# Kernel tuning notes

Hardware: AMD Instinct MI355X
Metric: run time of the kernel (lower is better)

The kernel has to match this reference:

```python
import jax, jax.numpy as jnp
import numpy as np

B, S, E = 4, 2048, 1024

def setup_inputs() -> dict:
    key = jax.random.key(0)
    ks = jax.random.split(key, 9)
    lim = 1.0 / np.sqrt(E)
    inp = {
        "query": jax.random.normal(ks[0], (B, S, E), dtype=jnp.float32),
        "key": jax.random.normal(ks[1], (B, S, E), dtype=jnp.float32),
        "value": jax.random.normal(ks[2], (B, S, E), dtype=jnp.float32),
        "Wq": jax.random.uniform(ks[3], (E, E), jnp.float32, -lim, lim),
        "bq": jax.random.uniform(ks[4], (E,), jnp.float32, -lim, lim),
        "Wk": jax.random.uniform(ks[5], (E, E), jnp.float32, -lim, lim),
        "bk": jax.random.uniform(ks[6], (E,), jnp.float32, -lim, lim),
        "Wv": jax.random.uniform(ks[7], (E, E), jnp.float32, -lim, lim),
        "bv": jax.random.uniform(ks[8], (E,), jnp.float32, -lim, lim),
    }
    return inp

def reference(query, key, value, Wq, bq, Wk, bk, Wv, bv):
    # Linear layers (torch stores weight as [out,in]; here W is [in,out] used as x @ W)
    q = query @ Wq + bq            # [B,S,E]
    k = key @ Wk + bk              # [B,S,E]
    v = value @ Wv + bv            # [B,S,E]
    inv_scale = jnp.asarray(E, q.dtype) ** 0.5
    scores = jnp.einsum("bse,bte->bst", q, k) / inv_scale  # [B,S,S]
    attn = jax.nn.softmax(scores, axis=-1)
    # dropout_p = 0.0 -> identity
    out = jnp.einsum("bst,bte->bse", attn, v)  # [B,S,E]
    return out
```

## Files before the change

kernel.cpp:

```cpp
#include <hip/hip_runtime.h>
#include <hip/hip_bf16.h>


typedef __bf16 bf16_t;
typedef bf16_t bf16x8 __attribute__((ext_vector_type(8)));
typedef bf16_t bf16x4 __attribute__((ext_vector_type(4)));
typedef float  f32x4  __attribute__((ext_vector_type(4)));

typedef const __attribute__((address_space(1))) unsigned gl_uint;
typedef __attribute__((address_space(3))) unsigned lds_uint;

#define BM 128
#define BN 128
#define BK 64

__device__ __forceinline__ void gload_lds16(const void* g, void* l) {
  __builtin_amdgcn_global_load_lds((gl_uint*)g, (lds_uint*)l, 16, 0, 0);
}

template <bool LSUM>
__device__ __forceinline__ void mfma_tile(const bf16_t* As, const bf16_t* Bs,
                                          f32x4 acc[4][4], f32x4 acc_l[4]) {
  const int lane = threadIdx.x & 63;
  const int quad = lane >> 4;
  const int l15  = lane & 15;
  const int wid  = threadIdx.x >> 6;
  const int wm   = (wid >> 1) * 64;
  const int wn   = (wid & 1) * 64;
  const int csw  = l15 & 7;
  bf16x8 ones;
  if (LSUM) {
#pragma unroll
    for (int t = 0; t < 8; ++t) ones[t] = (bf16_t)1.0f;
  }
#pragma unroll
  for (int ks = 0; ks < 2; ++ks) {
    const int sg = ks * 4 + quad;
    const int c  = (sg ^ csw) * 8;
    bf16x8 fa[4], fb[4];
#pragma unroll
    for (int i = 0; i < 4; ++i)
      fa[i] = *(const bf16x8*)&As[(wm + i * 16 + l15) * BK + c];
#pragma unroll
    for (int i = 0; i < 4; ++i)
      fb[i] = *(const bf16x8*)&Bs[(wn + i * 16 + l15) * BK + c];
#pragma unroll
    for (int mi = 0; mi < 4; ++mi)
#pragma unroll
      for (int ni = 0; ni < 4; ++ni)
        acc[mi][ni] = __builtin_amdgcn_mfma_f32_16x16x32_bf16(
            fa[mi], fb[ni], acc[mi][ni], 0, 0, 0);
    if (LSUM) {
#pragma unroll
      for (int mi = 0; mi < 4; ++mi)
        acc_l[mi] = __builtin_amdgcn_mfma_f32_16x16x32_bf16(
            fa[mi], ones, acc_l[mi], 0, 0, 0);
    }
  }
}

template <bool LSUM>
__device__ __forceinline__ void gemm_core_bf16(
    const bf16_t* __restrict__ Ab, const bf16_t* __restrict__ Bb,
    const int K, bf16_t* As, bf16_t* Bs, f32x4 acc[4][4], f32x4 acc_l[4])
{
  const int tid = threadIdx.x;
  for (int kt = 0; kt < K; kt += BK) {
#pragma unroll
    for (int j = 0; j < 4; ++j) {
      const int lin = j * 256 + tid;
      const int row = lin >> 3;
      const int seg = (lin & 7) ^ (row & 7);
      gload_lds16(Ab + (size_t)row * K + kt + seg * 8, &As[lin * 8]);
    }
#pragma unroll
    for (int j = 0; j < 4; ++j) {
      const int lin = j * 256 + tid;
      const int row = lin >> 3;
      const int seg = (lin & 7) ^ (row & 7);
      gload_lds16(Bb + (size_t)row * K + kt + seg * 8, &Bs[lin * 8]);
    }
    __syncthreads();
    mfma_tile<LSUM>(As, Bs, acc, acc_l);
    __syncthreads();
  }
}

__global__ __launch_bounds__(256, 2)
void qkv_proj(const bf16_t* __restrict__ qb, const bf16_t* __restrict__ kb,
              const bf16_t* __restrict__ vb, const bf16_t* __restrict__ Wqt,
              const bf16_t* __restrict__ Wkt, const bf16_t* __restrict__ Wvt,
              const float* __restrict__ bq, const float* __restrict__ bk,
              const float* __restrict__ bv, bf16_t* __restrict__ qp,
              bf16_t* __restrict__ kp, bf16_t* __restrict__ vT)
{
  __shared__ __align__(16) bf16_t As[BM * BK];
  __shared__ __align__(16) bf16_t Bs[BN * BK];

  const int L = blockIdx.x;
  const int g = L >> 3;
  const int gst = (L & 7) * 3 + (g >> 6);
  const int z  = gst >> 3;
  const int sy = gst & 7;
  const int w  = g & 63;
  const int bx = w & 7;
  const int by = sy * 8 + (w >> 3);

  const bf16_t* A    = (z == 0) ? qb : (z == 1) ? kb : vb;
  const bf16_t* W    = (z == 0) ? Wqt : (z == 1) ? Wkt : Wvt;
  const float*  bias = (z == 0) ? bq : (z == 1) ? bk : bv;
  const int K = 1024, N = 1024;
  const bf16_t* Ab = A + (size_t)by * BM * K;
  const bf16_t* Bb = W + (size_t)bx * BN * K;

  f32x4 acc[4][4];
  const f32x4 z4 = {0.f, 0.f, 0.f, 0.f};
#pragma unroll
  for (int i = 0; i < 4; ++i)
#pragma unroll
    for (int j = 0; j < 4; ++j) acc[i][j] = z4;

  gemm_core_bf16<false>(Ab, Bb, K, As, Bs, acc, nullptr);

  const int lane = threadIdx.x & 63;
  const int quad = lane >> 4;
  const int l15  = lane & 15;
  const int wid  = threadIdx.x >> 6;
  const int wm = (wid >> 1) * 64, wn = (wid & 1) * 64;
  const int m0 = by * BM, n0 = bx * BN;
#pragma unroll
  for (int mi = 0; mi < 4; ++mi) {
#pragma unroll
    for (int ni = 0; ni < 4; ++ni) {
      const int gn = n0 + wn + ni * 16 + l15;
      const int gm = m0 + wm + mi * 16 + quad * 4;
      const float bv_ = bias[gn];
      f32x4 a = acc[mi][ni];
      if (z < 2) {
        bf16_t* C = (z == 0) ? qp : kp;
#pragma unroll
        for (int r = 0; r < 4; ++r)
          C[(size_t)(gm + r) * N + gn] = (bf16_t)(a[r] + bv_);
      } else {
        const int b = gm >> 11;
        const int s = gm & 2047;
        bf16x4 o;
#pragma unroll
        for (int r = 0; r < 4; ++r) o[r] = (bf16_t)(a[r] + bv_);
        *(bf16x4*)&vT[((size_t)b * N + gn) * 2048 + s] = o;
      }
    }
  }
}

template <int MODE>
__global__ __launch_bounds__(256, 2)
void gemm_att(const bf16_t* __restrict__ A, const bf16_t* __restrict__ Bt,
              void* __restrict__ Cv,
              const int M, const int N, const int K,
              const long long sA, const long long sB, const long long sC)
{
  __shared__ __align__(16) bf16_t As[BM * BK];
  __shared__ __align__(16) bf16_t Bs[BN * BK];

  const int L = blockIdx.x;
  int bx, by, bz;
  if (MODE == 0) {
    const int g = L >> 3;
    const int gst = (L & 7) * 2 + (g >> 6);
    bz = gst >> 2;
    const int s2 = gst & 3;
    const int w = g & 63;
    bx = (s2 & 1) * 8 + (w & 7);
    by = (s2 >> 1) * 8 + (w >> 3);
  } else {
    const int xcd = L & 7;
    const int w = (L >> 3) & 63;
    bz = xcd >> 1;
    bx = w & 7;
    by = (xcd & 1) * 8 + (w >> 3);
  }

  const bf16_t* Ab = A + (size_t)bz * sA + (size_t)by * BM * K;
  const bf16_t* Bb = Bt + (size_t)bz * sB + (size_t)bx * BN * K;

  f32x4 acc[4][4];
  f32x4 acc_l[4];
  const f32x4 z4 = {0.f, 0.f, 0.f, 0.f};
#pragma unroll
  for (int i = 0; i < 4; ++i) {
    acc_l[i] = z4;
#pragma unroll
    for (int j = 0; j < 4; ++j) acc[i][j] = z4;
  }

  gemm_core_bf16<MODE == 1>(Ab, Bb, K, As, Bs, acc, acc_l);

  const int lane = threadIdx.x & 63;
  const int quad = lane >> 4;
  const int l15  = lane & 15;
  const int wid  = threadIdx.x >> 6;
  const int wm = (wid >> 1) * 64, wn = (wid & 1) * 64;
  const int m0 = by * BM, n0 = bx * BN;

  if (MODE == 0) {
    const float cexp = 0.03125f * 1.4426950408889634f;
    bf16_t* C = (bf16_t*)Cv + (size_t)bz * sC;
#pragma unroll
    for (int mi = 0; mi < 4; ++mi) {
      const int gm = m0 + wm + mi * 16 + quad * 4;
#pragma unroll
      for (int ni = 0; ni < 4; ++ni) {
        const int gn = n0 + wn + ni * 16 + l15;
        f32x4 a = acc[mi][ni];
#pragma unroll
        for (int r = 0; r < 4; ++r)
          C[(size_t)(gm + r) * N + gn] = (bf16_t)exp2f(a[r] * cexp);
      }
    }
  } else {
    float* C = (float*)Cv + (size_t)bz * sC;
#pragma unroll
    for (int mi = 0; mi < 4; ++mi) {
      const int gm = m0 + wm + mi * 16 + quad * 4;
      float il[4];
#pragma unroll
      for (int r = 0; r < 4; ++r) il[r] = 1.0f / acc_l[mi][r];
#pragma unroll
      for (int ni = 0; ni < 4; ++ni) {
        const int gn = n0 + wn + ni * 16 + l15;
        f32x4 a = acc[mi][ni];
#pragma unroll
        for (int r = 0; r < 4; ++r)
          C[(size_t)(gm + r) * N + gn] = a[r] * il[r];
      }
    }
  }
}

__global__ __launch_bounds__(256)
void prep(const float* __restrict__ q, const float* __restrict__ k,
          const float* __restrict__ v, const float* __restrict__ Wq,
          const float* __restrict__ Wk, const float* __restrict__ Wv,
          bf16_t* __restrict__ qo, bf16_t* __restrict__ ko,
          bf16_t* __restrict__ vo, bf16_t* __restrict__ Wqt,
          bf16_t* __restrict__ Wkt, bf16_t* __restrict__ Wvt) {
  const int L = blockIdx.x;
  const int tid = threadIdx.x;
  if (L < 24576) {
    const int z = L >> 13;
    const int blk = L & 8191;
    const float* in = (z == 0) ? q : (z == 1) ? k : v;
    bf16_t* out = (z == 0) ? qo : (z == 1) ? ko : vo;
    const size_t i = ((size_t)blk * 256 + tid) * 4;
    const float4 w = *(const float4*)(in + i);
    bf16x4 o;
    o[0] = (bf16_t)w.x; o[1] = (bf16_t)w.y; o[2] = (bf16_t)w.z; o[3] = (bf16_t)w.w;
    *(bf16x4*)(out + i) = o;
  } else {
    const int t = L - 24576;
    const int z = t >> 8;
    const int wi = t & 255;
    const float* W = (z == 0) ? Wq : (z == 1) ? Wk : Wv;
    bf16_t* Wt = (z == 0) ? Wqt : (z == 1) ? Wkt : Wvt;
    __shared__ float tile[64][65];
    const int n0 = (wi & 15) * 64;
    const int k0 = (wi >> 4) * 64;
#pragma unroll
    for (int it = 0; it < 16; ++it) {
      const int idx = it * 256 + tid;
      const int r = idx >> 6, c = idx & 63;
      tile[r][c] = W[(size_t)(k0 + r) * 1024 + n0 + c];
    }
    __syncthreads();
#pragma unroll
    for (int it = 0; it < 16; ++it) {
      const int idx = it * 256 + tid;
      const int r = idx >> 6, c = idx & 63;
      Wt[(size_t)(n0 + r) * 1024 + k0 + c] = (bf16_t)tile[c][r];
    }
  }
}

extern "C" void kernel_launch(void* const* d_in, const int* in_sizes, int n_in,
                              void* d_out, int out_size, void* d_ws, size_t ws_size,
                              hipStream_t stream) {
  const int B = 4, S = 2048, E = 1024;
  const size_t BSE = (size_t)B * S * E;
  const size_t EE  = (size_t)E * E;

  const float* q_in = (const float*)d_in[0];
  const float* k_in = (const float*)d_in[1];
  const float* v_in = (const float*)d_in[2];
  const float* Wq = (const float*)d_in[3];
  const float* bq = (const float*)d_in[4];
  const float* Wk = (const float*)d_in[5];
  const float* bk = (const float*)d_in[6];
  const float* Wv = (const float*)d_in[7];
  const float* bv = (const float*)d_in[8];
  float* out = (float*)d_out;

  char* ws = (char*)d_ws;
  bf16_t* Wqt = (bf16_t*)ws;
  bf16_t* Wkt = Wqt + EE;
  bf16_t* Wvt = Wkt + EE;
  bf16_t* qb  = Wvt + EE;
  bf16_t* kb  = qb + BSE;
  bf16_t* vb  = kb + BSE;
  bf16_t* qp  = vb + BSE;
  bf16_t* kp  = qp + BSE;
  bf16_t* vT  = kp + BSE;
  bf16_t* P   = vT + BSE;

  prep<<<25344, 256, 0, stream>>>(q_in, k_in, v_in, Wq, Wk, Wv,
                                  qb, kb, vb, Wqt, Wkt, Wvt);

  qkv_proj<<<1536, 256, 0, stream>>>(qb, kb, vb, Wqt, Wkt, Wvt,
                                     bq, bk, bv, qp, kp, vT);

  gemm_att<0><<<1024, 256, 0, stream>>>(
      qp, kp, P, S, S, E,
      (long long)S * E, (long long)S * E, (long long)S * S);

  gemm_att<1><<<512, 256, 0, stream>>>(
      P, vT, out, S, E, S,
      (long long)S * S, (long long)E * S, (long long)S * E);

  (void)in_sizes; (void)n_in; (void)out_size; (void)ws_size;
}
```

Before: 285.1 us.

## Use 256x256 eight-wave pipelined GEMM for QKV projection and scores

Adds a 256x256-tile GEMM core for 8 waves. It double-buffers LDS with direct global-to-LDS loads, uses explicit vmcnt waits, barriers and setprio so loads overlap the MFMA phases. The QKV projection and score kernels switch to this core with fewer, larger blocks, and the scores epilogue writes exp2 of the scaled scores directly to P. Larger tiles raise data reuse and cut global traffic, but they use more registers and 128KB of LDS, and a smaller grid risks poorer load balance across CUs. The scores epilogue has no max subtraction, so it relies on the score range staying small enough for exp without overflow.

```diff
diff --git a/kernel.cpp b/kernel.cpp
--- a/kernel.cpp
+++ b/kernel.cpp
@@ -16,6 +16,231 @@
 
 __device__ __forceinline__ void gload_lds16(const void* g, void* l) {
   __builtin_amdgcn_global_load_lds((gl_uint*)g, (lds_uint*)l, 16, 0, 0);
+}
+
+#define VMCNT(N) asm volatile("s_waitcnt vmcnt(" #N ")" ::: "memory")
+#define LGKM0()  asm volatile("s_waitcnt lgkmcnt(0)" ::: "memory")
+
+__device__ __forceinline__ void gemm256_8p(
+    const bf16_t* __restrict__ Ab, const bf16_t* __restrict__ Bb,
+    const int K, bf16_t* Lb, f32x4 acc[8][4])
+{
+  const int tid  = threadIdx.x;
+  const int lane = tid & 63;
+  const int l15  = lane & 15;
+  const int quad = lane >> 4;
+  const int wid  = tid >> 6;
+  const int wr   = wid >> 2;
+  const int wc   = wid & 3;
+  const int swz0 = (quad ^ (l15 & 7)) * 8;
+  const int swz1 = ((quad + 4) ^ (l15 & 7)) * 8;
+
+  const int r0  = tid >> 3, r1 = r0 + 64;
+  const int so0 = r0 * K + (((tid & 7) ^ (r0 & 7)) * 8);
+  const int so1 = r1 * K + (((tid & 7) ^ (r1 & 7)) * 8);
+  const int sd0 = tid * 8, sd1 = 4096 + tid * 8;
+
+#define HALF(buf, h) (Lb + ((buf) * 4 + (h)) * 8192)
+#define STAGE(gsrc, buf, h) { const bf16_t* _g = (gsrc); bf16_t* _l = HALF(buf, h); \
+    gload_lds16(_g + so0, _l + sd0); gload_lds16(_g + so1, _l + sd1); }
+
+  const int aoff = l15 * 64;
+  const int boff = ((wc & 1) * 64 + l15) * 64;
+  bf16x8 fa[4][2], fb[4][2];
+
+#define RD_FB(buf) { const bf16_t* _B = HALF(buf, 2 + (wc >> 1)) + boff; \
+  _Pragma("unroll") for (int ni = 0; ni < 4; ++ni) { \
+    fb[ni][0] = *(const bf16x8*)(_B + ni * 1024 + swz0); \
+    fb[ni][1] = *(const bf16x8*)(_B + ni * 1024 + swz1); } }
+#define RD_FA(buf, MO) { const bf16_t* _A = HALF(buf, wr) + aoff + (MO) * 1024; \
+  _Pragma("unroll") for (int mi = 0; mi < 4; ++mi) { \
+    fa[mi][0] = *(const bf16x8*)(_A + mi * 1024 + swz0); \
+    fa[mi][1] = *(const bf16x8*)(_A + mi * 1024 + swz1); } }
+
+#define MFQ(MH, NL) \
+  _Pragma("unroll") for (int kk = 0; kk < 2; ++kk) \
+  _Pragma("unroll") for (int mi = 0; mi < 4; ++mi) \
+  _Pragma("unroll") for (int ni = 0; ni < 2; ++ni) \
+    acc[(MH) * 4 + mi][(NL) + ni] = __builtin_amdgcn_mfma_f32_16x16x32_bf16( \
+        fa[mi][kk], fb[(NL) + ni][kk], acc[(MH) * 4 + mi][(NL) + ni], 0, 0, 0);
+
+#define PH_PRE() __builtin_amdgcn_s_barrier(); LGKM0(); \
+                 __builtin_amdgcn_sched_barrier(0); __builtin_amdgcn_s_setprio(1)
+#define PH_POST() __builtin_amdgcn_s_setprio(0); __builtin_amdgcn_sched_barrier(0)
+
+  const int NJ = K >> 7;
+  const size_t hk = (size_t)128 * K;
+
+  STAGE(Bb,           0, 2);  STAGE(Bb + hk,      0, 3);
+  STAGE(Ab,           0, 0);  STAGE(Ab + hk,      0, 1);
+  STAGE(Bb + 64,      1, 2);  STAGE(Bb + hk + 64, 1, 3);
+  STAGE(Ab + 64,      1, 0);
+  VMCNT(6);
+  __builtin_amdgcn_s_barrier();
+
+  for (int j = 0; j < NJ - 1; ++j) {
+    const int c1 = 2 * j * 64 + 64;
+    const int c2 = c1 + 64, c3 = c2 + 64;
+    RD_FB(0); RD_FA(0, 0);
+    STAGE(Ab + hk + c1, 1, 1);
+    PH_PRE(); MFQ(0, 0); PH_POST(); __builtin_amdgcn_s_barrier();
+    STAGE(Bb + c2, 0, 2);
+    PH_PRE(); MFQ(0, 2); PH_POST(); __builtin_amdgcn_s_barrier();
+    RD_FA(0, 4);
+    STAGE(Bb + hk + c2, 0, 3);
+    PH_PRE(); MFQ(1, 0); PH_POST(); __builtin_amdgcn_s_barrier();
+    STAGE(Ab + c2, 0, 0);
+    PH_PRE(); MFQ(1, 2); PH_POST(); VMCNT(6); __builtin_amdgcn_s_barrier();
+    RD_FB(1); RD_FA(1, 0);
+    STAGE(Ab + hk + c2, 0, 1);
+    PH_PRE(); MFQ(0, 0); PH_POST(); __builtin_amdgcn_s_barrier();
+    STAGE(Bb + c3, 1, 2);
+    PH_PRE(); MFQ(0, 2); PH_POST(); __builtin_amdgcn_s_barrier();
+    RD_FA(1, 4);
+    STAGE(Bb + hk + c3, 1, 3);
+    PH_PRE(); MFQ(1, 0); PH_POST(); __builtin_amdgcn_s_barrier();
+    STAGE(Ab + c3, 1, 0);
+    PH_PRE(); MFQ(1, 2); PH_POST(); VMCNT(6); __builtin_amdgcn_s_barrier();
+  }
+  {
+    const int c1 = K - 64;
+    RD_FB(0); RD_FA(0, 0);
+    STAGE(Ab + hk + c1, 1, 1);
+    PH_PRE(); MFQ(0, 0); PH_POST(); __builtin_amdgcn_s_barrier();
+    PH_PRE(); MFQ(0, 2); PH_POST(); __builtin_amdgcn_s_barrier();
+    RD_FA(0, 4);
+    PH_PRE(); MFQ(1, 0); PH_POST(); __builtin_amdgcn_s_barrier();
+    PH_PRE(); MFQ(1, 2); PH_POST(); VMCNT(0); __builtin_amdgcn_s_barrier();
+    RD_FB(1); RD_FA(1, 0);
+    PH_PRE(); MFQ(0, 0); PH_POST(); __builtin_amdgcn_s_barrier();
+    PH_PRE(); MFQ(0, 2); PH_POST(); __builtin_amdgcn_s_barrier();
+    RD_FA(1, 4);
+    PH_PRE(); MFQ(1, 0); PH_POST(); __builtin_amdgcn_s_barrier();
+    PH_PRE(); MFQ(1, 2); PH_POST();
+  }
+#undef HALF
+#undef STAGE
+#undef RD_FB
+#undef RD_FA
+#undef MFQ
+#undef PH_PRE
+#undef PH_POST
+}
+
+__global__ __launch_bounds__(512, 2)
+void qkv_proj8(const bf16_t* __restrict__ qb, const bf16_t* __restrict__ kb,
+               const bf16_t* __restrict__ vb, const bf16_t* __restrict__ Wqt,
+               const bf16_t* __restrict__ Wkt, const bf16_t* __restrict__ Wvt,
+               const float* __restrict__ bq, const float* __restrict__ bk,
+               const float* __restrict__ bv, bf16_t* __restrict__ qp,
+               bf16_t* __restrict__ kp, bf16_t* __restrict__ vT)
+{
+  __shared__ __align__(16) bf16_t lds[2 * 4 * 8192];
+  const int L   = blockIdx.x;
+  const int lin = (L & 7) * 48 + (L >> 3);
+  const int z   = lin >> 7;
+  const int r   = lin & 127;
+  const int by  = r >> 2, bx = r & 3;
+  const int K = 1024, N = 1024;
+
+  const bf16_t* A    = (z == 0) ? qb : (z == 1) ? kb : vb;
+  const bf16_t* W    = (z == 0) ? Wqt : (z == 1) ? Wkt : Wvt;
+  const float*  bias = (z == 0) ? bq : (z == 1) ? bk : bv;
+
+  f32x4 acc[8][4];
+  const f32x4 z4 = {0.f, 0.f, 0.f, 0.f};
+#pragma unroll
+  for (int i = 0; i < 8; ++i)
+#pragma unroll
+    for (int jj = 0; jj < 4; ++jj) acc[i][jj] = z4;
+
+  gemm256_8p(A + (size_t)by * 256 * K, W + (size_t)bx * 256 * K, K, lds, acc);
+
+  const int tid = threadIdx.x;
+  const int lane = tid & 63, l15 = lane & 15, quad = lane >> 4;
+  const int wid = tid >> 6, wr = wid >> 2, wc = wid & 3;
+  const int m0 = by * 256 + wr * 128;
+  const int n0 = bx * 256 + wc * 64;
+  float bv_[4];
+#pragma unroll
+  for (int ni = 0; ni < 4; ++ni) bv_[ni] = bias[n0 + ni * 16 + l15];
+
+  if (z < 2) {
+    bf16_t* C = (z == 0) ? qp : kp;
+#pragma unroll
+    for (int mi = 0; mi < 8; ++mi) {
+      const int gm = m0 + mi * 16 + quad * 4;
+#pragma unroll
+      for (int ni = 0; ni < 4; ++ni) {
+        const int gn = n0 + ni * 16 + l15;
+        f32x4 a = acc[mi][ni];
+#pragma unroll
+        for (int rr = 0; rr < 4; ++rr)
+          C[(size_t)(gm + rr) * N + gn] = (bf16_t)(a[rr] + bv_[ni]);
+      }
+    }
+  } else {
+#pragma unroll
+    for (int mi = 0; mi < 8; ++mi) {
+      const int gm = m0 + mi * 16 + quad * 4;
+      const int b = gm >> 11;
+      const int s = gm & 2047;
+#pragma unroll
+      for (int ni = 0; ni < 4; ++ni) {
+        const int gn = n0 + ni * 16 + l15;
+        f32x4 a = acc[mi][ni];
+        bf16x4 o;
+#pragma unroll
+        for (int rr = 0; rr < 4; ++rr) o[rr] = (bf16_t)(a[rr] + bv_[ni]);
+        *(bf16x4*)&vT[((size_t)b * N + gn) * 2048 + s] = o;
+      }
+    }
+  }
+}
+
+__global__ __launch_bounds__(512, 2)
+void scores8(const bf16_t* __restrict__ qp, const bf16_t* __restrict__ kp,
+             bf16_t* __restrict__ P)
+{
+  __shared__ __align__(16) bf16_t lds[2 * 4 * 8192];
+  const int L   = blockIdx.x;
+  const int lin = (L & 7) * 32 + (L >> 3);
+  const int bz  = lin >> 6;
+  const int r   = lin & 63;
+  const int by  = r >> 3, bx = r & 7;
+  const int K = 1024;
+
+  const bf16_t* Ab = qp + (size_t)bz * 2048 * 1024 + (size_t)by * 256 * K;
+  const bf16_t* Bb = kp + (size_t)bz * 2048 * 1024 + (size_t)bx * 256 * K;
+
+  f32x4 acc[8][4];
+  const f32x4 z4 = {0.f, 0.f, 0.f, 0.f};
+#pragma unroll
+  for (int i = 0; i < 8; ++i)
+#pragma unroll
+    for (int jj = 0; jj < 4; ++jj) acc[i][jj] = z4;
+
+  gemm256_8p(Ab, Bb, K, lds, acc);
+
+  const int tid = threadIdx.x;
+  const int lane = tid & 63, l15 = lane & 15, quad = lane >> 4;
+  const int wid = tid >> 6, wr = wid >> 2, wc = wid & 3;
+  const int m0 = by * 256 + wr * 128;
+  const int n0 = bx * 256 + wc * 64;
+  bf16_t* C = P + (size_t)bz * 2048 * 2048;
+  const float cexp = 0.03125f * 1.4426950408889634f;
+#pragma unroll
+  for (int mi = 0; mi < 8; ++mi) {
+    const int gm = m0 + mi * 16 + quad * 4;
+#pragma unroll
+    for (int ni = 0; ni < 4; ++ni) {
+      const int gn = n0 + ni * 16 + l15;
+      f32x4 a = acc[mi][ni];
+#pragma unroll
+      for (int rr = 0; rr < 4; ++rr)
+        C[(size_t)(gm + rr) * 2048 + gn] = (bf16_t)exp2f(a[rr] * cexp);
+    }
+  }
 }
 
 template <bool LSUM>
@@ -83,73 +308,6 @@
     __syncthreads();
     mfma_tile<LSUM>(As, Bs, acc, acc_l);
     __syncthreads();
-  }
-}
-
-__global__ __launch_bounds__(256, 2)
-void qkv_proj(const bf16_t* __restrict__ qb, const bf16_t* __restrict__ kb,
-              const bf16_t* __restrict__ vb, const bf16_t* __restrict__ Wqt,
-              const bf16_t* __restrict__ Wkt, const bf16_t* __restrict__ Wvt,
-              const float* __restrict__ bq, const float* __restrict__ bk,
-              const float* __restrict__ bv, bf16_t* __restrict__ qp,
-              bf16_t* __restrict__ kp, bf16_t* __restrict__ vT)
-{
-  __shared__ __align__(16) bf16_t As[BM * BK];
-  __shared__ __align__(16) bf16_t Bs[BN * BK];
-
-  const int L = blockIdx.x;
-  const int g = L >> 3;
-  const int gst = (L & 7) * 3 + (g >> 6);
-  const int z  = gst >> 3;
-  const int sy = gst & 7;
-  const int w  = g & 63;
-  const int bx = w & 7;
-  const int by = sy * 8 + (w >> 3);
-
-  const bf16_t* A    = (z == 0) ? qb : (z == 1) ? kb : vb;
-  const bf16_t* W    = (z == 0) ? Wqt : (z == 1) ? Wkt : Wvt;
-  const float*  bias = (z == 0) ? bq : (z == 1) ? bk : bv;
-  const int K = 1024, N = 1024;
-  const bf16_t* Ab = A + (size_t)by * BM * K;
-  const bf16_t* Bb = W + (size_t)bx * BN * K;
-
-  f32x4 acc[4][4];
-  const f32x4 z4 = {0.f, 0.f, 0.f, 0.f};
-#pragma unroll
-  for (int i = 0; i < 4; ++i)
-#pragma unroll
-    for (int j = 0; j < 4; ++j) acc[i][j] = z4;
-
-  gemm_core_bf16<false>(Ab, Bb, K, As, Bs, acc, nullptr);
-
-  const int lane = threadIdx.x & 63;
-  const int quad = lane >> 4;
-  const int l15  = lane & 15;
-  const int wid  = threadIdx.x >> 6;
-  const int wm = (wid >> 1) * 64, wn = (wid & 1) * 64;
-  const int m0 = by * BM, n0 = bx * BN;
-#pragma unroll
-  for (int mi = 0; mi < 4; ++mi) {
-#pragma unroll
-    for (int ni = 0; ni < 4; ++ni) {
-      const int gn = n0 + wn + ni * 16 + l15;
-      const int gm = m0 + wm + mi * 16 + quad * 4;
-      const float bv_ = bias[gn];
-      f32x4 a = acc[mi][ni];
-      if (z < 2) {
-        bf16_t* C = (z == 0) ? qp : kp;
-#pragma unroll
-        for (int r = 0; r < 4; ++r)
-          C[(size_t)(gm + r) * N + gn] = (bf16_t)(a[r] + bv_);
-      } else {
-        const int b = gm >> 11;
-        const int s = gm & 2047;
-        bf16x4 o;
-#pragma unroll
-        for (int r = 0; r < 4; ++r) o[r] = (bf16_t)(a[r] + bv_);
-        *(bf16x4*)&vT[((size_t)b * N + gn) * 2048 + s] = o;
-      }
-    }
   }
 }
 
@@ -315,12 +473,10 @@
   prep<<<25344, 256, 0, stream>>>(q_in, k_in, v_in, Wq, Wk, Wv,
                                   qb, kb, vb, Wqt, Wkt, Wvt);
 
-  qkv_proj<<<1536, 256, 0, stream>>>(qb, kb, vb, Wqt, Wkt, Wvt,
+  qkv_proj8<<<384, 512, 0, stream>>>(qb, kb, vb, Wqt, Wkt, Wvt,
                                      bq, bk, bv, qp, kp, vT);
 
-  gemm_att<0><<<1024, 256, 0, stream>>>(
-      qp, kp, P, S, S, E,
-      (long long)S * E, (long long)S * E, (long long)S * S);
+  scores8<<<256, 512, 0, stream>>>(qp, kp, P);
 
   gemm_att<1><<<512, 256, 0, stream>>>(
       P, vT, out, S, E, S,
```

After: 296.3 us. +3.9%, slower.

## Replace QKV and score GEMMs with triple-buffered 256x128 pipelined kernels

Applied to the files above, without the earlier changes.

Adds a new GEMM core that uses 512-thread blocks on a 256x128 tile, with three LDS stages filled by async global-to-LDS loads. Explicit vmcnt waits and barriers let loads for later k-tiles overlap the MFMA work, and register fragments are double-buffered between LDS reads and MFMAs. Both the QKV projection and the QK^T score kernel now use this core; the score kernel's exp epilogue (scale and exp2) is carried over from the old MODE 0 path. The cost is much more LDS per block (about 144 KB), which may limit occupancy, plus hand-tuned wait counts that are fragile.

```diff
diff --git a/kernel.cpp b/kernel.cpp
--- a/kernel.cpp
+++ b/kernel.cpp
@@ -16,6 +16,206 @@
 
 __device__ __forceinline__ void gload_lds16(const void* g, void* l) {
   __builtin_amdgcn_global_load_lds((gl_uint*)g, (lds_uint*)l, 16, 0, 0);
+}
+
+#define VMCNT(N) asm volatile("s_waitcnt vmcnt(" #N ")" ::: "memory")
+#define LGKM0()  asm volatile("s_waitcnt lgkmcnt(0)" ::: "memory")
+
+__device__ __forceinline__ void gemm_v3(
+    const bf16_t* __restrict__ Ab, const bf16_t* __restrict__ Bb,
+    bf16_t* Lb, f32x4 acc[4][4])
+{
+  const int tid  = threadIdx.x;
+  const int lane = tid & 63;
+  const int l15  = lane & 15;
+  const int quad = lane >> 4;
+  const int wid  = tid >> 6;
+  const int wr   = wid >> 1;
+  const int wcl  = wid & 1;
+  const int swz0 = (quad ^ (l15 & 7)) * 8;
+  const int swz1 = ((quad + 4) ^ (l15 & 7)) * 8;
+
+  const int r8 = tid >> 3, s8 = tid & 7;
+  const size_t gbase = (size_t)r8 * 1024 + (size_t)((s8 ^ (r8 & 7)) * 8);
+  const int dbase = tid * 8;
+
+#define SLOTA(s) (Lb + (s) * 24576)
+#define SLOTB(s) (Lb + (s) * 24576 + 16384)
+#define STAGE6(ktile, slot) { \
+    const bf16_t* _A = Ab + (size_t)(ktile) * 64; \
+    const bf16_t* _B = Bb + (size_t)(ktile) * 64; \
+    bf16_t* _la = SLOTA(slot); bf16_t* _lb = SLOTB(slot); \
+    gload_lds16(_A + gbase,                     _la + dbase); \
+    gload_lds16(_A + gbase + (size_t)64 * 1024, _la + dbase + 4096); \
+    gload_lds16(_A + gbase + (size_t)128 * 1024, _la + dbase + 8192); \
+    gload_lds16(_A + gbase + (size_t)192 * 1024, _la + dbase + 12288); \
+    gload_lds16(_B + gbase,                     _lb + dbase); \
+    gload_lds16(_B + gbase + (size_t)64 * 1024, _lb + dbase + 4096); }
+
+  const int aoff = (wr * 64 + l15) * 64;
+  const int boff = (wcl * 64 + l15) * 64;
+
+#define RD(slot, FA, FB) { \
+    const bf16_t* _a = SLOTA(slot) + aoff; \
+    const bf16_t* _b = SLOTB(slot) + boff; \
+    _Pragma("unroll") for (int mi = 0; mi < 4; ++mi) { \
+      FA[mi][0] = *(const bf16x8*)(_a + mi * 1024 + swz0); \
+      FA[mi][1] = *(const bf16x8*)(_a + mi * 1024 + swz1); } \
+    _Pragma("unroll") for (int ni = 0; ni < 4; ++ni) { \
+      FB[ni][0] = *(const bf16x8*)(_b + ni * 1024 + swz0); \
+      FB[ni][1] = *(const bf16x8*)(_b + ni * 1024 + swz1); } }
+
+#define MFM(FA, FB) \
+    _Pragma("unroll") for (int kk = 0; kk < 2; ++kk) \
+    _Pragma("unroll") for (int mi = 0; mi < 4; ++mi) \
+    _Pragma("unroll") for (int ni = 0; ni < 4; ++ni) \
+      acc[mi][ni] = __builtin_amdgcn_mfma_f32_16x16x32_bf16( \
+          FA[mi][kk], FB[ni][kk], acc[mi][ni], 0, 0, 0);
+
+  bf16x8 fa0[4][2], fb0[4][2], fa1[4][2], fb1[4][2];
+
+  STAGE6(0, 0); STAGE6(1, 1); STAGE6(2, 2);
+  VMCNT(6);
+  __builtin_amdgcn_s_barrier();
+  RD(0, fa0, fb0);
+  LGKM0();
+  __builtin_amdgcn_s_barrier();
+
+#pragma unroll
+  for (int kt = 0; kt < 14; ++kt) {
+    const int ss = kt % 3;
+    const int rs = (kt + 1) % 3;
+    if (kt <= 12) STAGE6(kt + 3, ss);
+    if ((kt & 1) == 0) { RD(rs, fa1, fb1); MFM(fa0, fb0); }
+    else               { RD(rs, fa0, fb0); MFM(fa1, fb1); }
+    if (kt <= 12) { VMCNT(6); }
+    else          { VMCNT(0); }
+    __builtin_amdgcn_s_barrier();
+  }
+  RD(0, fa1, fb1); MFM(fa0, fb0);
+  MFM(fa1, fb1);
+
+#undef SLOTA
+#undef SLOTB
+#undef STAGE6
+#undef RD
+#undef MFM
+}
+
+__global__ __launch_bounds__(512, 2)
+void qkv_v3(const bf16_t* __restrict__ qb, const bf16_t* __restrict__ kb,
+            const bf16_t* __restrict__ vb, const bf16_t* __restrict__ Wqt,
+            const bf16_t* __restrict__ Wkt, const bf16_t* __restrict__ Wvt,
+            const float* __restrict__ bq, const float* __restrict__ bk,
+            const float* __restrict__ bv, bf16_t* __restrict__ qp,
+            bf16_t* __restrict__ kp, bf16_t* __restrict__ vT)
+{
+  __shared__ __align__(16) bf16_t lds[3 * 24576];
+  const int L   = blockIdx.x;
+  const int lin = (L & 7) * 96 + (L >> 3);
+  const int z   = lin >> 8;
+  const int r   = lin & 255;
+  const int by  = r >> 3, bx = r & 7;
+  const int K = 1024, N = 1024;
+
+  const bf16_t* A    = (z == 0) ? qb : (z == 1) ? kb : vb;
+  const bf16_t* W    = (z == 0) ? Wqt : (z == 1) ? Wkt : Wvt;
+  const float*  bias = (z == 0) ? bq : (z == 1) ? bk : bv;
+
+  f32x4 acc[4][4];
+  const f32x4 z4 = {0.f, 0.f, 0.f, 0.f};
+#pragma unroll
+  for (int i = 0; i < 4; ++i)
+#pragma unroll
+    for (int j = 0; j < 4; ++j) acc[i][j] = z4;
+
+  gemm_v3(A + (size_t)by * 256 * K, W + (size_t)bx * 128 * K, lds, acc);
+
+  const int tid = threadIdx.x;
+  const int lane = tid & 63, l15 = lane & 15, quad = lane >> 4;
+  const int wid = tid >> 6, wr = wid >> 1, wcl = wid & 1;
+  const int m0 = by * 256 + wr * 64;
+  const int n0 = bx * 128 + wcl * 64;
+  float bv_[4];
+#pragma unroll
+  for (int ni = 0; ni < 4; ++ni) bv_[ni] = bias[n0 + ni * 16 + l15];
+
+  if (z < 2) {
+    bf16_t* C = (z == 0) ? qp : kp;
+#pragma unroll
+    for (int mi = 0; mi < 4; ++mi) {
+      const int gm = m0 + mi * 16 + quad * 4;
+#pragma unroll
+      for (int ni = 0; ni < 4; ++ni) {
+        const int gn = n0 + ni * 16 + l15;
+        f32x4 a = acc[mi][ni];
+#pragma unroll
+        for (int rr = 0; rr < 4; ++rr)
+          C[(size_t)(gm + rr) * N + gn] = (bf16_t)(a[rr] + bv_[ni]);
+      }
+    }
+  } else {
+#pragma unroll
+    for (int mi = 0; mi < 4; ++mi) {
+      const int gm = m0 + mi * 16 + quad * 4;
+      const int b = gm >> 11;
+      const int s = gm & 2047;
+#pragma unroll
+      for (int ni = 0; ni < 4; ++ni) {
+        const int gn = n0 + ni * 16 + l15;
+        f32x4 a = acc[mi][ni];
+        bf16x4 o;
+#pragma unroll
+        for (int rr = 0; rr < 4; ++rr) o[rr] = (bf16_t)(a[rr] + bv_[ni]);
+        *(bf16x4*)&vT[((size_t)b * N + gn) * 2048 + s] = o;
+      }
+    }
+  }
+}
+
+__global__ __launch_bounds__(512, 2)
+void scores_v3(const bf16_t* __restrict__ qp, const bf16_t* __restrict__ kp,
+               bf16_t* __restrict__ P)
+{
+  __shared__ __align__(16) bf16_t lds[3 * 24576];
+  const int L   = blockIdx.x;
+  const int lin = (L & 7) * 64 + (L >> 3);
+  const int bz  = lin >> 7;
+  const int r   = lin & 127;
+  const int by  = r >> 4, bx = r & 15;
+  const int K = 1024;
+
+  const bf16_t* Ab = qp + (size_t)bz * 2048 * 1024 + (size_t)by * 256 * K;
+  const bf16_t* Bb = kp + (size_t)bz * 2048 * 1024 + (size_t)bx * 128 * K;
+
+  f32x4 acc[4][4];
+  const f32x4 z4 = {0.f, 0.f, 0.f, 0.f};
+#pragma unroll
+  for (int i = 0; i < 4; ++i)
+#pragma unroll
+    for (int j = 0; j < 4; ++j) acc[i][j] = z4;
+
+  gemm_v3(Ab, Bb, lds, acc);
+
+  const int tid = threadIdx.x;
+  const int lane = tid & 63, l15 = lane & 15, quad = lane >> 4;
+  const int wid = tid >> 6, wr = wid >> 1, wcl = wid & 1;
+  const int m0 = by * 256 + wr * 64;
+  const int n0 = bx * 128 + wcl * 64;
+  bf16_t* C = P + (size_t)bz * 2048 * 2048;
+  const float cexp = 0.03125f * 1.4426950408889634f;
+#pragma unroll
+  for (int mi = 0; mi < 4; ++mi) {
+    const int gm = m0 + mi * 16 + quad * 4;
+#pragma unroll
+    for (int ni = 0; ni < 4; ++ni) {
+      const int gn = n0 + ni * 16 + l15;
+      f32x4 a = acc[mi][ni];
+#pragma unroll
+      for (int rr = 0; rr < 4; ++rr)
+        C[(size_t)(gm + rr) * 2048 + gn] = (bf16_t)exp2f(a[rr] * cexp);
+    }
+  }
 }
 
 template <bool LSUM>
@@ -83,73 +283,6 @@
     __syncthreads();
     mfma_tile<LSUM>(As, Bs, acc, acc_l);
     __syncthreads();
-  }
-}
-
-__global__ __launch_bounds__(256, 2)
-void qkv_proj(const bf16_t* __restrict__ qb, const bf16_t* __restrict__ kb,
-              const bf16_t* __restrict__ vb, const bf16_t* __restrict__ Wqt,
-              const bf16_t* __restrict__ Wkt, const bf16_t* __restrict__ Wvt,
-              const float* __restrict__ bq, const float* __restrict__ bk,
-              const float* __restrict__ bv, bf16_t* __restrict__ qp,
-              bf16_t* __restrict__ kp, bf16_t* __restrict__ vT)
-{
-  __shared__ __align__(16) bf16_t As[BM * BK];
-  __shared__ __align__(16) bf16_t Bs[BN * BK];
-
-  const int L = blockIdx.x;
-  const int g = L >> 3;
-  const int gst = (L & 7) * 3 + (g >> 6);
-  const int z  = gst >> 3;
-  const int sy = gst & 7;
-  const int w  = g & 63;
-  const int bx = w & 7;
-  const int by = sy * 8 + (w >> 3);
-
-  const bf16_t* A    = (z == 0) ? qb : (z == 1) ? kb : vb;
-  const bf16_t* W    = (z == 0) ? Wqt : (z == 1) ? Wkt : Wvt;
-  const float*  bias = (z == 0) ? bq : (z == 1) ? bk : bv;
-  const int K = 1024, N = 1024;
-  const bf16_t* Ab = A + (size_t)by * BM * K;
-  const bf16_t* Bb = W + (size_t)bx * BN * K;
-
-  f32x4 acc[4][4];
-  const f32x4 z4 = {0.f, 0.f, 0.f, 0.f};
-#pragma unroll
-  for (int i = 0; i < 4; ++i)
-#pragma unroll
-    for (int j = 0; j < 4; ++j) acc[i][j] = z4;
-
-  gemm_core_bf16<false>(Ab, Bb, K, As, Bs, acc, nullptr);
-
-  const int lane = threadIdx.x & 63;
-  const int quad = lane >> 4;
-  const int l15  = lane & 15;
-  const int wid  = threadIdx.x >> 6;
-  const int wm = (wid >> 1) * 64, wn = (wid & 1) * 64;
-  const int m0 = by * BM, n0 = bx * BN;
-#pragma unroll
-  for (int mi = 0; mi < 4; ++mi) {
-#pragma unroll
-    for (int ni = 0; ni < 4; ++ni) {
-      const int gn = n0 + wn + ni * 16 + l15;
-      const int gm = m0 + wm + mi * 16 + quad * 4;
-      const float bv_ = bias[gn];
-      f32x4 a = acc[mi][ni];
-      if (z < 2) {
-        bf16_t* C = (z == 0) ? qp : kp;
-#pragma unroll
-        for (int r = 0; r < 4; ++r)
-          C[(size_t)(gm + r) * N + gn] = (bf16_t)(a[r] + bv_);
-      } else {
-        const int b = gm >> 11;
-        const int s = gm & 2047;
-        bf16x4 o;
-#pragma unroll
-        for (int r = 0; r < 4; ++r) o[r] = (bf16_t)(a[r] + bv_);
-        *(bf16x4*)&vT[((size_t)b * N + gn) * 2048 + s] = o;
-      }
-    }
   }
 }
 
@@ -315,12 +448,10 @@
   prep<<<25344, 256, 0, stream>>>(q_in, k_in, v_in, Wq, Wk, Wv,
                                   qb, kb, vb, Wqt, Wkt, Wvt);
 
-  qkv_proj<<<1536, 256, 0, stream>>>(qb, kb, vb, Wqt, Wkt, Wvt,
-                                     bq, bk, bv, qp, kp, vT);
-
-  gemm_att<0><<<1024, 256, 0, stream>>>(
-      qp, kp, P, S, S, E,
-      (long long)S * E, (long long)S * E, (long long)S * S);
+  qkv_v3<<<768, 512, 0, stream>>>(qb, kb, vb, Wqt, Wkt, Wvt,
+                                  bq, bk, bv, qp, kp, vT);
+
+  scores_v3<<<512, 512, 0, stream>>>(qp, kp, P);
 
   gemm_att<1><<<512, 256, 0, stream>>>(
       P, vT, out, S, E, S,
```

Result: no change. 284.0 us (-0.4%).

## Fuse all four stages into one persistent kernel with grid barriers

Applied to the files above, without the earlier changes.

Replaces the four kernel launches (prep, QKV projection, scores+exp, PV GEMM) with a single persistent kernel of 512 blocks. The blocks loop over the old tile indices and synchronise between stages with atomic-counter grid barriers that use explicit L2 writeback and invalidate fences. This removes launch gaps and tail effects between kernels. In exchange it adds a memset launch and spin-wait barrier cost, and it relies on all 512 blocks being co-resident at two blocks per CU.

```diff
diff --git a/kernel.cpp b/kernel.cpp
--- a/kernel.cpp
+++ b/kernel.cpp
@@ -13,14 +13,37 @@
 #define BM 128
 #define BN 128
 #define BK 64
+#define NBLK 512u
 
 __device__ __forceinline__ void gload_lds16(const void* g, void* l) {
   __builtin_amdgcn_global_load_lds((gl_uint*)g, (lds_uint*)l, 16, 0, 0);
 }
 
+__device__ __forceinline__ void fence_release() {
+  asm volatile("s_waitcnt vmcnt(0) lgkmcnt(0)" ::: "memory");
+  asm volatile("buffer_wbl2 sc1" ::: "memory");
+  asm volatile("s_waitcnt vmcnt(0)" ::: "memory");
+}
+__device__ __forceinline__ void fence_acquire() {
+  asm volatile("buffer_inv sc1" ::: "memory");
+}
+
+__device__ __forceinline__ void grid_barrier(unsigned* ctr) {
+  __syncthreads();
+  if (threadIdx.x == 0) {
+    fence_release();
+    __threadfence();
+    atomicAdd(ctr, 1u);
+    while (atomicAdd(ctr, 0u) < NBLK) { __builtin_amdgcn_s_sleep(8); }
+    __threadfence();
+    fence_acquire();
+  }
+  __syncthreads();
+}
+
 template <bool LSUM>
-__device__ __forceinline__ void mfma_tile(const bf16_t* As, const bf16_t* Bs,
-                                          f32x4 acc[4][4], f32x4 acc_l[4]) {
+__device__ __forceinline__ void mfma_tile128(const bf16_t* As, const bf16_t* Bs,
+                                             f32x4 acc[4][4], f32x4 acc_l[4]) {
   const int lane = threadIdx.x & 63;
   const int quad = lane >> 4;
   const int l15  = lane & 15;
@@ -60,7 +83,7 @@
 }
 
 template <bool LSUM>
-__device__ __forceinline__ void gemm_core_bf16(
+__device__ __forceinline__ void gemm_core128(
     const bf16_t* __restrict__ Ab, const bf16_t* __restrict__ Bb,
     const int K, bf16_t* As, bf16_t* Bs, f32x4 acc[4][4], f32x4 acc_l[4])
 {
@@ -81,131 +104,165 @@
       gload_lds16(Bb + (size_t)row * K + kt + seg * 8, &Bs[lin * 8]);
     }
     __syncthreads();
-    mfma_tile<LSUM>(As, Bs, acc, acc_l);
+    mfma_tile128<LSUM>(As, Bs, acc, acc_l);
     __syncthreads();
   }
 }
 
 __global__ __launch_bounds__(256, 2)
-void qkv_proj(const bf16_t* __restrict__ qb, const bf16_t* __restrict__ kb,
-              const bf16_t* __restrict__ vb, const bf16_t* __restrict__ Wqt,
-              const bf16_t* __restrict__ Wkt, const bf16_t* __restrict__ Wvt,
-              const float* __restrict__ bq, const float* __restrict__ bk,
-              const float* __restrict__ bv, bf16_t* __restrict__ qp,
-              bf16_t* __restrict__ kp, bf16_t* __restrict__ vT)
+void fused_all(const float* __restrict__ q_in, const float* __restrict__ k_in,
+               const float* __restrict__ v_in, const float* __restrict__ Wq,
+               const float* __restrict__ Wk, const float* __restrict__ Wv,
+               const float* __restrict__ bq, const float* __restrict__ bk,
+               const float* __restrict__ bv,
+               bf16_t* __restrict__ qb, bf16_t* __restrict__ kb,
+               bf16_t* __restrict__ vb, bf16_t* __restrict__ Wqt,
+               bf16_t* __restrict__ Wkt, bf16_t* __restrict__ Wvt,
+               bf16_t* __restrict__ qp, bf16_t* __restrict__ kp,
+               bf16_t* __restrict__ vT, bf16_t* __restrict__ P,
+               float* __restrict__ out, unsigned* __restrict__ ctrs)
 {
-  __shared__ __align__(16) bf16_t As[BM * BK];
-  __shared__ __align__(16) bf16_t Bs[BN * BK];
-
-  const int L = blockIdx.x;
-  const int g = L >> 3;
-  const int gst = (L & 7) * 3 + (g >> 6);
-  const int z  = gst >> 3;
-  const int sy = gst & 7;
-  const int w  = g & 63;
-  const int bx = w & 7;
-  const int by = sy * 8 + (w >> 3);
-
-  const bf16_t* A    = (z == 0) ? qb : (z == 1) ? kb : vb;
-  const bf16_t* W    = (z == 0) ? Wqt : (z == 1) ? Wkt : Wvt;
-  const float*  bias = (z == 0) ? bq : (z == 1) ? bk : bv;
-  const int K = 1024, N = 1024;
-  const bf16_t* Ab = A + (size_t)by * BM * K;
-  const bf16_t* Bb = W + (size_t)bx * BN * K;
-
-  f32x4 acc[4][4];
-  const f32x4 z4 = {0.f, 0.f, 0.f, 0.f};
-#pragma unroll
-  for (int i = 0; i < 4; ++i)
-#pragma unroll
-    for (int j = 0; j < 4; ++j) acc[i][j] = z4;
-
-  gemm_core_bf16<false>(Ab, Bb, K, As, Bs, acc, nullptr);
-
-  const int lane = threadIdx.x & 63;
-  const int quad = lane >> 4;
-  const int l15  = lane & 15;
-  const int wid  = threadIdx.x >> 6;
-  const int wm = (wid >> 1) * 64, wn = (wid & 1) * 64;
-  const int m0 = by * BM, n0 = bx * BN;
-#pragma unroll
-  for (int mi = 0; mi < 4; ++mi) {
-#pragma unroll
-    for (int ni = 0; ni < 4; ++ni) {
-      const int gn = n0 + wn + ni * 16 + l15;
-      const int gm = m0 + wm + mi * 16 + quad * 4;
-      const float bv_ = bias[gn];
-      f32x4 a = acc[mi][ni];
-      if (z < 2) {
-        bf16_t* C = (z == 0) ? qp : kp;
-#pragma unroll
-        for (int r = 0; r < 4; ++r)
-          C[(size_t)(gm + r) * N + gn] = (bf16_t)(a[r] + bv_);
-      } else {
-        const int b = gm >> 11;
-        const int s = gm & 2047;
-        bf16x4 o;
-#pragma unroll
-        for (int r = 0; r < 4; ++r) o[r] = (bf16_t)(a[r] + bv_);
-        *(bf16x4*)&vT[((size_t)b * N + gn) * 2048 + s] = o;
-      }
-    }
-  }
-}
-
-template <int MODE>
-__global__ __launch_bounds__(256, 2)
-void gemm_att(const bf16_t* __restrict__ A, const bf16_t* __restrict__ Bt,
-              void* __restrict__ Cv,
-              const int M, const int N, const int K,
-              const long long sA, const long long sB, const long long sC)
-{
-  __shared__ __align__(16) bf16_t As[BM * BK];
-  __shared__ __align__(16) bf16_t Bs[BN * BK];
-
-  const int L = blockIdx.x;
-  int bx, by, bz;
-  if (MODE == 0) {
+  __shared__ __align__(16) char smem[32768];
+  bf16_t* As = (bf16_t*)smem;
+  bf16_t* Bs = As + BM * BK;
+  const int bid = blockIdx.x;
+  const int tid = threadIdx.x;
+
+  {
+    const float* src[3] = {q_in, k_in, v_in};
+    bf16_t*      dst[3] = {qb, kb, vb};
+#pragma unroll 1
+    for (int it = 0; it < 48; ++it) {
+      const size_t i4  = ((size_t)it * 512 + bid) * 256 + tid;
+      const int    z   = (int)(i4 >> 21);
+      const size_t off = (i4 & 2097151) * 4;
+      const float4 w = *(const float4*)(src[z] + off);
+      bf16x4 o;
+      o[0] = (bf16_t)w.x; o[1] = (bf16_t)w.y;
+      o[2] = (bf16_t)w.z; o[3] = (bf16_t)w.w;
+      *(bf16x4*)(dst[z] + off) = o;
+    }
+    float (*tile)[65] = (float(*)[65])smem;
+#pragma unroll 1
+    for (int t = bid; t < 768; t += 512) {
+      const int z = t >> 8;
+      const int wi = t & 255;
+      const float* W = (z == 0) ? Wq : (z == 1) ? Wk : Wv;
+      bf16_t* Wt = (z == 0) ? Wqt : (z == 1) ? Wkt : Wvt;
+      const int n0 = (wi & 15) * 64;
+      const int k0 = (wi >> 4) * 64;
+      __syncthreads();
+#pragma unroll
+      for (int itr = 0; itr < 16; ++itr) {
+        const int idx = itr * 256 + tid;
+        const int r = idx >> 6, c = idx & 63;
+        tile[r][c] = W[(size_t)(k0 + r) * 1024 + n0 + c];
+      }
+      __syncthreads();
+#pragma unroll
+      for (int itr = 0; itr < 16; ++itr) {
+        const int idx = itr * 256 + tid;
+        const int r = idx >> 6, c = idx & 63;
+        Wt[(size_t)(n0 + r) * 1024 + k0 + c] = (bf16_t)tile[c][r];
+      }
+    }
+    __syncthreads();
+  }
+
+  grid_barrier(ctrs + 0);
+
+#pragma unroll 1
+  for (int rr = 0; rr < 3; ++rr) {
+    const int L = bid + rr * 512;
+    const int g = L >> 3;
+    const int gst = (L & 7) * 3 + (g >> 6);
+    const int z  = gst >> 3;
+    const int sy = gst & 7;
+    const int w  = g & 63;
+    const int bx = w & 7;
+    const int by = sy * 8 + (w >> 3);
+
+    const bf16_t* A    = (z == 0) ? qb : (z == 1) ? kb : vb;
+    const bf16_t* W    = (z == 0) ? Wqt : (z == 1) ? Wkt : Wvt;
+    const float*  bias = (z == 0) ? bq : (z == 1) ? bk : bv;
+    const int K = 1024, N = 1024;
+    const bf16_t* Ab = A + (size_t)by * BM * K;
+    const bf16_t* Bb = W + (size_t)bx * BN * K;
+
+    f32x4 acc[4][4];
+    const f32x4 z4 = {0.f, 0.f, 0.f, 0.f};
+#pragma unroll
+    for (int i = 0; i < 4; ++i)
+#pragma unroll
+      for (int j = 0; j < 4; ++j) acc[i][j] = z4;
+
+    gemm_core128<false>(Ab, Bb, K, As, Bs, acc, nullptr);
+
+    const int lane = tid & 63;
+    const int quad = lane >> 4;
+    const int l15  = lane & 15;
+    const int wid  = tid >> 6;
+    const int wm = (wid >> 1) * 64, wn = (wid & 1) * 64;
+    const int m0 = by * BM, n0 = bx * BN;
+#pragma unroll
+    for (int mi = 0; mi < 4; ++mi) {
+#pragma unroll
+      for (int ni = 0; ni < 4; ++ni) {
+        const int gn = n0 + wn + ni * 16 + l15;
+        const int gm = m0 + wm + mi * 16 + quad * 4;
+        const float bv_ = bias[gn];
+        f32x4 a = acc[mi][ni];
+        if (z < 2) {
+          bf16_t* C = (z == 0) ? qp : kp;
+#pragma unroll
+          for (int r = 0; r < 4; ++r)
+            C[(size_t)(gm + r) * N + gn] = (bf16_t)(a[r] + bv_);
+        } else {
+          const int b = gm >> 11;
+          const int s = gm & 2047;
+          bf16x4 o;
+#pragma unroll
+          for (int r = 0; r < 4; ++r) o[r] = (bf16_t)(a[r] + bv_);
+          *(bf16x4*)&vT[((size_t)b * N + gn) * 2048 + s] = o;
+        }
+      }
+    }
+  }
+
+  grid_barrier(ctrs + 16);
+
+#pragma unroll 1
+  for (int rr = 0; rr < 2; ++rr) {
+    const int L = bid + rr * 512;
     const int g = L >> 3;
     const int gst = (L & 7) * 2 + (g >> 6);
-    bz = gst >> 2;
+    const int bz = gst >> 2;
     const int s2 = gst & 3;
     const int w = g & 63;
-    bx = (s2 & 1) * 8 + (w & 7);
-    by = (s2 >> 1) * 8 + (w >> 3);
-  } else {
-    const int xcd = L & 7;
-    const int w = (L >> 3) & 63;
-    bz = xcd >> 1;
-    bx = w & 7;
-    by = (xcd & 1) * 8 + (w >> 3);
-  }
-
-  const bf16_t* Ab = A + (size_t)bz * sA + (size_t)by * BM * K;
-  const bf16_t* Bb = Bt + (size_t)bz * sB + (size_t)bx * BN * K;
-
-  f32x4 acc[4][4];
-  f32x4 acc_l[4];
-  const f32x4 z4 = {0.f, 0.f, 0.f, 0.f};
-#pragma unroll
-  for (int i = 0; i < 4; ++i) {
-    acc_l[i] = z4;
-#pragma unroll
-    for (int j = 0; j < 4; ++j) acc[i][j] = z4;
-  }
-
-  gemm_core_bf16<MODE == 1>(Ab, Bb, K, As, Bs, acc, acc_l);
-
-  const int lane = threadIdx.x & 63;
-  const int quad = lane >> 4;
-  const int l15  = lane & 15;
-  const int wid  = threadIdx.x >> 6;
-  const int wm = (wid >> 1) * 64, wn = (wid & 1) * 64;
-  const int m0 = by * BM, n0 = bx * BN;
-
-  if (MODE == 0) {
+    const int bx = (s2 & 1) * 8 + (w & 7);
+    const int by = (s2 >> 1) * 8 + (w >> 3);
+    const int K = 1024;
+
+    const bf16_t* Ab = qp + (size_t)bz * 2048 * 1024 + (size_t)by * BM * K;
+    const bf16_t* Bb = kp + (size_t)bz * 2048 * 1024 + (size_t)bx * BN * K;
+
+    f32x4 acc[4][4];
+    const f32x4 z4 = {0.f, 0.f, 0.f, 0.f};
+#pragma unroll
+    for (int i = 0; i < 4; ++i)
+#pragma unroll
+      for (int j = 0; j < 4; ++j) acc[i][j] = z4;
+
+    gemm_core128<false>(Ab, Bb, K, As, Bs, acc, nullptr);
+
+    const int lane = tid & 63;
+    const int quad = lane >> 4;
+    const int l15  = lane & 15;
+    const int wid  = tid >> 6;
+    const int wm = (wid >> 1) * 64, wn = (wid & 1) * 64;
+    const int m0 = by * BM, n0 = bx * BN;
+    bf16_t* C = P + (size_t)bz * 2048 * 2048;
     const float cexp = 0.03125f * 1.4426950408889634f;
-    bf16_t* C = (bf16_t*)Cv + (size_t)bz * sC;
 #pragma unroll
     for (int mi = 0; mi < 4; ++mi) {
       const int gm = m0 + wm + mi * 16 + quad * 4;
@@ -215,11 +272,43 @@
         f32x4 a = acc[mi][ni];
 #pragma unroll
         for (int r = 0; r < 4; ++r)
-          C[(size_t)(gm + r) * N + gn] = (bf16_t)exp2f(a[r] * cexp);
-      }
-    }
-  } else {
-    float* C = (float*)Cv + (size_t)bz * sC;
+          C[(size_t)(gm + r) * 2048 + gn] = (bf16_t)exp2f(a[r] * cexp);
+      }
+    }
+  }
+
+  grid_barrier(ctrs + 32);
+
+  {
+    const int L = bid;
+    const int xcd = L & 7;
+    const int w = (L >> 3) & 63;
+    const int bz = xcd >> 1;
+    const int bx = w & 7;
+    const int by = (xcd & 1) * 8 + (w >> 3);
+
+    const bf16_t* Ab = P  + (size_t)bz * 2048 * 2048 + (size_t)by * BM * 2048;
+    const bf16_t* Bb = vT + (size_t)bz * 1024 * 2048 + (size_t)bx * BN * 2048;
+
+    f32x4 acc[4][4];
+    f32x4 acc_l[4];
+    const f32x4 z4 = {0.f, 0.f, 0.f, 0.f};
+#pragma unroll
+    for (int i = 0; i < 4; ++i) {
+      acc_l[i] = z4;
+#pragma unroll
+      for (int j = 0; j < 4; ++j) acc[i][j] = z4;
+    }
+
+    gemm_core128<true>(Ab, Bb, 2048, As, Bs, acc, acc_l);
+
+    const int lane = tid & 63;
+    const int quad = lane >> 4;
+    const int l15  = lane & 15;
+    const int wid  = tid >> 6;
+    const int wm = (wid >> 1) * 64, wn = (wid & 1) * 64;
+    const int m0 = by * BM, n0 = bx * BN;
+    float* C = out + (size_t)bz * 2048 * 1024;
 #pragma unroll
     for (int mi = 0; mi < 4; ++mi) {
       const int gm = m0 + wm + mi * 16 + quad * 4;
@@ -232,52 +321,8 @@
         f32x4 a = acc[mi][ni];
 #pragma unroll
         for (int r = 0; r < 4; ++r)
-          C[(size_t)(gm + r) * N + gn] = a[r] * il[r];
-      }
-    }
-  }
-}
-
-__global__ __launch_bounds__(256)
-void prep(const float* __restrict__ q, const float* __restrict__ k,
-          const float* __restrict__ v, const float* __restrict__ Wq,
-          const float* __restrict__ Wk, const float* __restrict__ Wv,
-          bf16_t* __restrict__ qo, bf16_t* __restrict__ ko,
-          bf16_t* __restrict__ vo, bf16_t* __restrict__ Wqt,
-          bf16_t* __restrict__ Wkt, bf16_t* __restrict__ Wvt) {
-  const int L = blockIdx.x;
-  const int tid = threadIdx.x;
-  if (L < 24576) {
-    const int z = L >> 13;
-    const int blk = L & 8191;
-    const float* in = (z == 0) ? q : (z == 1) ? k : v;
-    bf16_t* out = (z == 0) ? qo : (z == 1) ? ko : vo;
-    const size_t i = ((size_t)blk * 256 + tid) * 4;
-    const float4 w = *(const float4*)(in + i);
-    bf16x4 o;
-    o[0] = (bf16_t)w.x; o[1] = (bf16_t)w.y; o[2] = (bf16_t)w.z; o[3] = (bf16_t)w.w;
-    *(bf16x4*)(out + i) = o;
-  } else {
-    const int t = L - 24576;
-    const int z = t >> 8;
-    const int wi = t & 255;
-    const float* W = (z == 0) ? Wq : (z == 1) ? Wk : Wv;
-    bf16_t* Wt = (z == 0) ? Wqt : (z == 1) ? Wkt : Wvt;
-    __shared__ float tile[64][65];
-    const int n0 = (wi & 15) * 64;
-    const int k0 = (wi >> 4) * 64;
-#pragma unroll
-    for (int it = 0; it < 16; ++it) {
-      const int idx = it * 256 + tid;
-      const int r = idx >> 6, c = idx & 63;
-      tile[r][c] = W[(size_t)(k0 + r) * 1024 + n0 + c];
-    }
-    __syncthreads();
-#pragma unroll
-    for (int it = 0; it < 16; ++it) {
-      const int idx = it * 256 + tid;
-      const int r = idx >> 6, c = idx & 63;
-      Wt[(size_t)(n0 + r) * 1024 + k0 + c] = (bf16_t)tile[c][r];
+          C[(size_t)(gm + r) * 1024 + gn] = a[r] * il[r];
+      }
     }
   }
 }
@@ -311,20 +356,13 @@
   bf16_t* kp  = qp + BSE;
   bf16_t* vT  = kp + BSE;
   bf16_t* P   = vT + BSE;
-
-  prep<<<25344, 256, 0, stream>>>(q_in, k_in, v_in, Wq, Wk, Wv,
-                                  qb, kb, vb, Wqt, Wkt, Wvt);
-
-  qkv_proj<<<1536, 256, 0, stream>>>(qb, kb, vb, Wqt, Wkt, Wvt,
-                                     bq, bk, bv, qp, kp, vT);
-
-  gemm_att<0><<<1024, 256, 0, stream>>>(
-      qp, kp, P, S, S, E,
-      (long long)S * E, (long long)S * E, (long long)S * S);
-
-  gemm_att<1><<<512, 256, 0, stream>>>(
-      P, vT, out, S, E, S,
-      (long long)S * S, (long long)E * S, (long long)S * E);
+  unsigned* ctrs = (unsigned*)(P + (size_t)B * S * S);
+
+  hipMemsetAsync(ctrs, 0, 48 * sizeof(unsigned), stream);
+
+  fused_all<<<512, 256, 0, stream>>>(q_in, k_in, v_in, Wq, Wk, Wv,
+                                     bq, bk, bv, qb, kb, vb,
+                                     Wqt, Wkt, Wvt, qp, kp, vT, P, out, ctrs);
 
   (void)in_sizes; (void)n_in; (void)out_size; (void)ws_size;
 }
```

Result: slower. 520.9 us (+82.7%).
